# Kernel optimization log

Measured on AMD Instinct MI355X. Metric: run time of the kernel, lower is better.

The kernel has to match this reference:

```python
import jax, jax.numpy as jnp
import numpy as np

INPUT_SIZE = 32      # activity vocab
HIDDEN = 128
OUTPUT = 33          # 32 act logits + 1 duration
NUM_LAYERS = 2
MAX_LEN = 256
SOS = 0


def setup_inputs() -> dict:
    key = jax.random.key(0)
    ks = jax.random.split(key, 16)
    s = 0.05
    inp = {
        "batch_size": 8192,
        "hidden": jax.random.normal(ks[0], (NUM_LAYERS, 8192, HIDDEN), jnp.float32),
        # CustomEmbedding: embed act index to hidden-1 dims, concat raw duration -> hidden dims
        "emb": jax.random.normal(ks[1], (INPUT_SIZE, HIDDEN - 1), jnp.float32) * s,
        # torch.nn.GRU params, gate order (r, z, n)
        "w_ih_0": jax.random.normal(ks[2], (3 * HIDDEN, HIDDEN), jnp.float32) * s,
        "w_hh_0": jax.random.normal(ks[3], (3 * HIDDEN, HIDDEN), jnp.float32) * s,
        "b_ih_0": jax.random.normal(ks[4], (3 * HIDDEN,), jnp.float32) * s,
        "b_hh_0": jax.random.normal(ks[5], (3 * HIDDEN,), jnp.float32) * s,
        "w_ih_1": jax.random.normal(ks[6], (3 * HIDDEN, HIDDEN), jnp.float32) * s,
        "w_hh_1": jax.random.normal(ks[7], (3 * HIDDEN, HIDDEN), jnp.float32) * s,
        "b_ih_1": jax.random.normal(ks[8], (3 * HIDDEN,), jnp.float32) * s,
        "b_hh_1": jax.random.normal(ks[9], (3 * HIDDEN,), jnp.float32) * s,
        "fc_w": jax.random.normal(ks[10], (OUTPUT, HIDDEN), jnp.float32) * s,
        "fc_b": jax.random.normal(ks[11], (OUTPUT,), jnp.float32) * s,
    }
    return inp


def _gru_cell(x, h, w_ih, w_hh, b_ih, b_hh):
    gi = x @ w_ih.T + b_ih          # [B, 3H]
    gh = h @ w_hh.T + b_hh
    ir, iz, inn = jnp.split(gi, 3, axis=-1)
    hr, hz, hn = jnp.split(gh, 3, axis=-1)
    r = jax.nn.sigmoid(ir + hr)
    z = jax.nn.sigmoid(iz + hz)
    n = jnp.tanh(inn + r * hn)
    return (1.0 - z) * n + z * h


def _decode(batch_size, hidden, emb, w_ih_0, w_hh_0, b_ih_0, b_hh_0,
            w_ih_1, w_hh_1, b_ih_1, b_hh_1, fc_w, fc_b):
    B = batch_size
    # decoder_input [B, 2]: (act_index_as_float, duration); sos index = 0
    init_inp = jnp.zeros((B, 2), hidden.dtype).at[:, 0].set(float(SOS))

    def step(carry, _):
        inp, h = carry
        act = inp[:, 0].astype(jnp.int32)
        x = jnp.concatenate([emb[act], inp[:, 1:2]], axis=-1)   # [B, H]
        h0 = _gru_cell(x, h[0], w_ih_0, w_hh_0, b_ih_0, b_hh_0)
        h1 = _gru_cell(h0, h[1], w_ih_1, w_hh_1, b_ih_1, b_hh_1)
        pred = h1 @ fc_w.T + fc_b                                # [B, O]
        # pack(): argmax over act logits; softmax over a size-1 seq dim == 1.0
        topi = jnp.argmax(pred[:, : OUTPUT - 1], axis=-1)
        nxt = jnp.concatenate(
            [topi.astype(pred.dtype)[:, None], jnp.ones((B, 1), pred.dtype)], axis=-1)
        return (nxt, jnp.stack([h0, h1])), pred

    _, outs = jax.lax.scan(step, (init_inp, hidden), None, length=MAX_LEN)
    outs = jnp.transpose(outs, (1, 0, 2))                        # [B, T, O]
    acts_logits = outs[..., : OUTPUT - 1]
    durations = jax.nn.softmax(outs[..., OUTPUT - 1:], axis=1)   # softmax over time
    log_probs = jnp.concatenate(
        [jax.nn.log_softmax(acts_logits, axis=-1), durations], axis=-1)
    probs = jnp.concatenate(
        [jax.nn.softmax(acts_logits, axis=-1), durations], axis=-1)
    return log_probs, probs


def reference(batch_size, hidden, emb, w_ih_0, w_hh_0, b_ih_0, b_hh_0,
              w_ih_1, w_hh_1, b_ih_1, b_hh_1, fc_w, fc_b):
    return _decode(batch_size, hidden, emb, w_ih_0, w_hh_0, b_ih_0, b_hh_0,
                   w_ih_1, w_hh_1, b_ih_1, b_hh_1, fc_w, fc_b)
```

## Files before the change

### kernel.cpp

```cpp
#include <hip/hip_runtime.h>

#define HDIM  128
#define G3    384
#define RPB   32
#define NTHR  512
#define NSTEP 256
#define NOUT  33
#define BROWS 8192
#define NBLK  (BROWS / RPB)
#define LOGP_ELEMS 69206016LL

typedef _Float16 half8 __attribute__((ext_vector_type(8)));
typedef float    f32x4 __attribute__((ext_vector_type(4)));

#define HS0_OFF   0
#define HS1_OFF   16384
#define BST_OFF   32768
#define FCL_OFF   131072
#define LDS_BYTES 155648

#define WP_BYTES  294912
#define FP_BYTES  24576

__device__ __forceinline__ float sigf(float x) { return 1.0f / (1.0f + __expf(-x)); }
__device__ __forceinline__ float tanh_fast(float x) { return 1.0f - 2.0f / (__expf(2.0f*x) + 1.0f); }

__global__ void prep_kernel(const float* __restrict__ emb, const float* __restrict__ wih0,
                            const float* __restrict__ bih0, float* __restrict__ T1,
                            float* __restrict__ T0) {
    int a = blockIdx.x;
    int g = threadIdx.x;
    const float* e = emb + a * 127;
    const float* w = wih0 + g * HDIM;
    float s = bih0[g];
    for (int k = 0; k < 127; ++k) s += e[k] * w[k];
    T1[a * G3 + g] = s + w[127];
    if (a == 0) T0[g] = s;
}

__global__ void prep_pack(const float* __restrict__ whh0, const float* __restrict__ wih1,
                          const float* __restrict__ whh1, const float* __restrict__ fcw,
                          half8* __restrict__ WP) {
    int b = blockIdx.x;
    int tid  = threadIdx.x;
    int lane = tid & 63;
    int kc   = tid >> 6;
    bool isfc = (b >= 72);
    if (!isfc) {
        int mat = b / 24, nt = b % 24;
        const float* W = (mat == 0) ? whh0 : (mat == 1) ? wih1 : whh1;
        int g = nt * 16 + (lane & 15);
        int k = kc * 32 + (lane >> 4) * 8;
        half8 v1;
#pragma unroll
        for (int e = 0; e < 8; ++e) v1[e] = (_Float16)W[g * HDIM + k + e];
        WP[(size_t)(((mat * 24 + nt) * 4 + kc)) * 64 + lane] = v1;
    } else {
        int nt = b - 72;
        int g = nt * 16 + (lane & 15);
        int k = kc * 32 + (lane >> 4) * 8;
        half8 v1, v2;
#pragma unroll
        for (int e = 0; e < 8; ++e) {
            float x = (g >= NOUT) ? 0.0f : fcw[g * HDIM + k + e];
            _Float16 s1 = (_Float16)x;
            v1[e] = s1; v2[e] = (_Float16)(x - (float)s1);
        }
        size_t base = (size_t)(WP_BYTES / 1024 + (nt * 4 + kc) * 2) * 64 + lane;
        WP[base]      = v1;
        WP[base + 64] = v2;
    }
}

__launch_bounds__(NTHR, 2)
__global__ void decoder_kernel(const float* __restrict__ hid,
                               const float* __restrict__ T1, const float* __restrict__ T0,
                               const char* __restrict__ Bpg,
                               const float* __restrict__ bhh0,
                               const float* __restrict__ bih1, const float* __restrict__ bhh1,
                               const float* __restrict__ fcb,
                               float* __restrict__ out) {
    extern __shared__ char smraw[];
    char*  hs0 = smraw + HS0_OFF;
    char*  hs1 = smraw + HS1_OFF;
    char*  bst = smraw + BST_OFF;
    char*  fcl = smraw + FCL_OFF;

    const int tid  = threadIdx.x;
    const int row0 = blockIdx.x * RPB;
    float* lp = out;
    float* pp = out + LOGP_ELEMS;

    const int lane  = tid & 63;
    const int w     = tid >> 6;
    const int col   = lane & 15;
    const int q     = lane >> 4;
    const int akoff = q * 16;
    const int j     = w * 16 + col;
    char* const mybuf = bst + (size_t)w * 12288;

    const float bG0 = bhh0[j],       bG1 = bhh0[128 + j], bG2 = bhh0[256 + j];
    const float bH0 = bhh1[j],       bH1 = bhh1[128 + j], bH2 = bhh1[256 + j];
    const float bI0 = bih1[j],       bI1 = bih1[128 + j], bI2 = bih1[256 + j];

    f32x4 fcbr[3];
#pragma unroll
    for (int t2 = 0; t2 < 3; ++t2)
#pragma unroll
        for (int i = 0; i < 4; ++i) {
            int o = 16 * t2 + q * 4 + i;
            fcbr[t2][i] = (o < NOUT) ? fcb[o] : 0.0f;
        }

    {
        const uint4* src = (const uint4*)(Bpg + WP_BYTES);
        uint4* dst = (uint4*)fcl;
        for (int i = tid; i < FP_BYTES / 16; i += NTHR) dst[i] = src[i];
    }

    float h0v[2][4], h1v[2][4];
#pragma unroll
    for (int Mt = 0; Mt < 2; ++Mt)
#pragma unroll
        for (int i = 0; i < 4; ++i) {
            int row = Mt * 16 + q * 4 + i;
            float v0 = hid[(size_t)(row0 + row) * HDIM + j];
            float v1 = hid[(size_t)BROWS * HDIM + (size_t)(row0 + row) * HDIM + j];
            h0v[Mt][i] = v0; h1v[Mt][i] = v1;
            int off = (row * 256 + j * 2) ^ ((row & 7) << 4);
            _Float16 s1 = (_Float16)v0, s2 = (_Float16)(v0 - (float)s1);
            *(_Float16*)(hs0 + off) = s1;
            *(_Float16*)(hs0 + 8192 + off) = s2;
            s1 = (_Float16)v1; s2 = (_Float16)(v1 - (float)s1);
            *(_Float16*)(hs1 + off) = s1;
            *(_Float16*)(hs1 + 8192 + off) = s2;
        }
    __syncthreads();

#define LGKM0() asm volatile("s_waitcnt lgkmcnt(0)" ::: "memory")
#define VMW()   asm volatile("s_waitcnt vmcnt(9)" ::: "memory")
#define BAR()   __builtin_amdgcn_s_barrier()
#define MFMA(a, b, c) __builtin_amdgcn_mfma_f32_16x16x32_f16((a), (b), (c), 0, 0, 0)

#define STAGE3(G_) do {                                                           \
        int gm_  = (G_) % 12;                                                     \
        int mat_ = (gm_ < 4) ? 0 : ((gm_ < 8) ? 2 : 1);                           \
        int kc_  = gm_ & 3;                                                       \
        char* db_ = mybuf + (size_t)(3 * ((G_) & 3)) * 1024;                      \
        _Pragma("unroll")                                                         \
        for (int ty_ = 0; ty_ < 3; ++ty_) {                                       \
            const char* src_ = Bpg + (size_t)(((mat_ * 24 + (ty_ * 8 + w)) * 4 + kc_) * 1024) + lane * 16; \
            __builtin_amdgcn_global_load_lds((const unsigned int*)src_,           \
                                             (unsigned int*)(db_ + ty_ * 1024), 16, 0, 0); \
        }                                                                         \
    } while (0)

#define GROUP(G_, HS_, ACC_) do {                                                 \
        STAGE3((G_) + 3);                                                         \
        VMW();                                                                    \
        int kc_ = (G_) & 3;                                                       \
        half8 a1_[2], a2_[2];                                                     \
        _Pragma("unroll")                                                         \
        for (int Mt_ = 0; Mt_ < 2; ++Mt_) {                                       \
            int row_ = Mt_ * 16 + col;                                            \
            int off_ = (row_ * 256 + kc_ * 64 + akoff) ^ ((row_ & 7) << 4);       \
            a1_[Mt_] = *(const half8*)((HS_) + off_);                             \
            a2_[Mt_] = *(const half8*)((HS_) + 8192 + off_);                      \
        }                                                                         \
        char* db_ = mybuf + (size_t)(3 * ((G_) & 3)) * 1024;                      \
        half8 b0_ = *(const half8*)(db_ + lane * 16);                             \
        half8 b1_ = *(const half8*)(db_ + 1024 + lane * 16);                      \
        half8 b2_ = *(const half8*)(db_ + 2048 + lane * 16);                      \
        _Pragma("unroll")                                                         \
        for (int Mt_ = 0; Mt_ < 2; ++Mt_) {                                       \
            ACC_[0][Mt_] = MFMA(a1_[Mt_], b0_, ACC_[0][Mt_]);                     \
            ACC_[0][Mt_] = MFMA(a2_[Mt_], b0_, ACC_[0][Mt_]);                     \
        }                                                                         \
        _Pragma("unroll")                                                         \
        for (int Mt_ = 0; Mt_ < 2; ++Mt_) {                                       \
            ACC_[1][Mt_] = MFMA(a1_[Mt_], b1_, ACC_[1][Mt_]);                     \
            ACC_[1][Mt_] = MFMA(a2_[Mt_], b1_, ACC_[1][Mt_]);                     \
        }                                                                         \
        _Pragma("unroll")                                                         \
        for (int Mt_ = 0; Mt_ < 2; ++Mt_) {                                       \
            ACC_[2][Mt_] = MFMA(a1_[Mt_], b2_, ACC_[2][Mt_]);                     \
            ACC_[2][Mt_] = MFMA(a2_[Mt_], b2_, ACC_[2][Mt_]);                     \
        }                                                                         \
    } while (0)

#define FC_SOFTMAX(TOUT_, ACTS_) do {                                             \
        f32x4 facc[2][3];                                                         \
        _Pragma("unroll")                                                         \
        for (int Mt_ = 0; Mt_ < 2; ++Mt_)                                         \
            _Pragma("unroll")                                                     \
            for (int t2_ = 0; t2_ < 3; ++t2_) facc[Mt_][t2_] = fcbr[t2_];         \
        _Pragma("unroll")                                                         \
        for (int kc_ = 0; kc_ < 4; ++kc_) {                                       \
            half8 a1_[2], a2_[2];                                                 \
            _Pragma("unroll")                                                     \
            for (int Mt_ = 0; Mt_ < 2; ++Mt_) {                                   \
                int row_ = Mt_ * 16 + col;                                        \
                int off_ = (row_ * 256 + kc_ * 64 + akoff) ^ ((row_ & 7) << 4);   \
                a1_[Mt_] = *(const half8*)(hs1 + off_);                           \
                a2_[Mt_] = *(const half8*)(hs1 + 8192 + off_);                    \
            }                                                                     \
            _Pragma("unroll")                                                     \
            for (int t2_ = 0; t2_ < 3; ++t2_) {                                   \
                half8 f1_ = *(const half8*)(fcl + ((t2_ * 4 + kc_) * 2 + 0) * 1024 + lane * 16); \
                half8 f2_ = *(const half8*)(fcl + ((t2_ * 4 + kc_) * 2 + 1) * 1024 + lane * 16); \
                _Pragma("unroll")                                                 \
                for (int Mt_ = 0; Mt_ < 2; ++Mt_) {                               \
                    facc[Mt_][t2_] = MFMA(f1_, a1_[Mt_], facc[Mt_][t2_]);         \
                    facc[Mt_][t2_] = MFMA(f1_, a2_[Mt_], facc[Mt_][t2_]);         \
                    facc[Mt_][t2_] = MFMA(f2_, a1_[Mt_], facc[Mt_][t2_]);         \
                }                                                                 \
            }                                                                     \
        }                                                                         \
        _Pragma("unroll")                                                         \
        for (int Mt_ = 0; Mt_ < 2; ++Mt_) {                                       \
            float bv_ = facc[Mt_][0][0]; int bi_ = q * 4;                         \
            _Pragma("unroll")                                                     \
            for (int t2_ = 0; t2_ < 2; ++t2_)                                     \
                _Pragma("unroll")                                                 \
                for (int i_ = 0; i_ < 4; ++i_) {                                  \
                    if (t2_ == 0 && i_ == 0) continue;                            \
                    float v_ = facc[Mt_][t2_][i_];                                \
                    int   o_ = 16 * t2_ + q * 4 + i_;                             \
                    if (v_ > bv_) { bv_ = v_; bi_ = o_; }                         \
                }                                                                 \
            _Pragma("unroll")                                                     \
            for (int d_ = 16; d_ <= 32; d_ <<= 1) {                               \
                float ov_ = __shfl_xor(bv_, d_);                                  \
                int   oi_ = __shfl_xor(bi_, d_);                                  \
                if (ov_ > bv_ || (ov_ == bv_ && oi_ < bi_)) { bv_ = ov_; bi_ = oi_; } \
            }                                                                     \
            (ACTS_)[Mt_] = bi_;                                                   \
            if (w == Mt_) {                                                       \
                float ex_[2][4]; float s_ = 0.0f;                                 \
                _Pragma("unroll")                                                 \
                for (int t2_ = 0; t2_ < 2; ++t2_)                                 \
                    _Pragma("unroll")                                             \
                    for (int i_ = 0; i_ < 4; ++i_) {                              \
                        ex_[t2_][i_] = __expf(facc[Mt_][t2_][i_] - bv_);          \
                        s_ += ex_[t2_][i_];                                       \
                    }                                                             \
                s_ += __shfl_xor(s_, 16);                                         \
                s_ += __shfl_xor(s_, 32);                                         \
                float ls_ = __logf(s_), inv_ = 1.0f / s_;                         \
                int r_ = lane & 15;                                               \
                size_t base_ = ((size_t)(row0 + Mt_ * 16 + r_) * NSTEP + (TOUT_)) * NOUT; \
                _Pragma("unroll")                                                 \
                for (int t2_ = 0; t2_ < 2; ++t2_)                                 \
                    _Pragma("unroll")                                             \
                    for (int i_ = 0; i_ < 4; ++i_) {                              \
                        int o_ = 16 * t2_ + q * 4 + i_;                           \
                        lp[base_ + o_] = facc[Mt_][t2_][i_] - bv_ - ls_;          \
                        pp[base_ + o_] = ex_[t2_][i_] * inv_;                     \
                    }                                                             \
                if (q == 0) lp[base_ + 32] = facc[Mt_][2][0];                     \
            }                                                                     \
        }                                                                         \
    } while (0)

    STAGE3(0); STAGE3(1); STAGE3(2);

#pragma unroll 1
    for (int t = 0; t < NSTEP; ++t) {
        float gi[3][2][4];
        if (t == 0) {
            float g0v = T0[j], g1v = T0[128 + j], g2v = T0[256 + j];
#pragma unroll
            for (int Mt = 0; Mt < 2; ++Mt)
#pragma unroll
                for (int i = 0; i < 4; ++i) {
                    gi[0][Mt][i] = g0v; gi[1][Mt][i] = g1v; gi[2][Mt][i] = g2v;
                }
        } else {
            int actsR[2];
            FC_SOFTMAX(t - 1, actsR);
#pragma unroll
            for (int Mt = 0; Mt < 2; ++Mt)
#pragma unroll
                for (int i = 0; i < 4; ++i) {
                    int act = __shfl(actsR[Mt], q * 4 + i);
                    const float* tab = T1 + act * G3;
                    gi[0][Mt][i] = tab[j];
                    gi[1][Mt][i] = tab[128 + j];
                    gi[2][Mt][i] = tab[256 + j];
                }
        }

        f32x4 g0[3][2], ah[3][2];
        {
            f32x4 v0 = {bG0, bG0, bG0, bG0}, v1 = {bG1, bG1, bG1, bG1}, v2 = {bG2, bG2, bG2, bG2};
            g0[0][0] = v0; g0[0][1] = v0; g0[1][0] = v1; g0[1][1] = v1; g0[2][0] = v2; g0[2][1] = v2;
            f32x4 u0 = {bH0, bH0, bH0, bH0}, u1 = {bH1, bH1, bH1, bH1}, u2 = {bH2, bH2, bH2, bH2};
            ah[0][0] = u0; ah[0][1] = u0; ah[1][0] = u1; ah[1][1] = u1; ah[2][0] = u2; ah[2][1] = u2;
        }
        GROUP(0, hs0, g0); GROUP(1, hs0, g0); GROUP(2, hs0, g0); GROUP(3, hs0, g0);
        GROUP(4, hs1, ah); GROUP(5, hs1, ah);

        _Float16 s1r[2][4], s2r[2][4];
#pragma unroll
        for (int Mt = 0; Mt < 2; ++Mt)
#pragma unroll
            for (int i = 0; i < 4; ++i) {
                float rg = sigf(gi[0][Mt][i] + g0[0][Mt][i]);
                float zg = sigf(gi[1][Mt][i] + g0[1][Mt][i]);
                float ng = tanh_fast(gi[2][Mt][i] + rg * g0[2][Mt][i]);
                float hnew = (1.0f - zg) * ng + zg * h0v[Mt][i];
                h0v[Mt][i] = hnew;
                s1r[Mt][i] = (_Float16)hnew;
                s2r[Mt][i] = (_Float16)(hnew - (float)s1r[Mt][i]);
            }

        GROUP(6, hs1, ah); GROUP(7, hs1, ah);
        LGKM0(); BAR();

#pragma unroll
        for (int Mt = 0; Mt < 2; ++Mt)
#pragma unroll
            for (int i = 0; i < 4; ++i) {
                int row = Mt * 16 + q * 4 + i;
                int off = (row * 256 + j * 2) ^ ((row & 7) << 4);
                *(_Float16*)(hs0 + off) = s1r[Mt][i];
                *(_Float16*)(hs0 + 8192 + off) = s2r[Mt][i];
            }
        LGKM0(); BAR();

        f32x4 ai[3][2];
        {
            f32x4 v0 = {bI0, bI0, bI0, bI0}, v1 = {bI1, bI1, bI1, bI1}, v2 = {bI2, bI2, bI2, bI2};
            ai[0][0] = v0; ai[0][1] = v0; ai[1][0] = v1; ai[1][1] = v1; ai[2][0] = v2; ai[2][1] = v2;
        }
        GROUP(8, hs0, ai); GROUP(9, hs0, ai); GROUP(10, hs0, ai); GROUP(11, hs0, ai);

#pragma unroll
        for (int Mt = 0; Mt < 2; ++Mt)
#pragma unroll
            for (int i = 0; i < 4; ++i) {
                float rg = sigf(ai[0][Mt][i] + ah[0][Mt][i]);
                float zg = sigf(ai[1][Mt][i] + ah[1][Mt][i]);
                float ng = tanh_fast(ai[2][Mt][i] + rg * ah[2][Mt][i]);
                float hnew = (1.0f - zg) * ng + zg * h1v[Mt][i];
                h1v[Mt][i] = hnew;
                int row = Mt * 16 + q * 4 + i;
                int off = (row * 256 + j * 2) ^ ((row & 7) << 4);
                _Float16 s1 = (_Float16)hnew, s2 = (_Float16)(hnew - (float)s1);
                *(_Float16*)(hs1 + off) = s1;
                *(_Float16*)(hs1 + 8192 + off) = s2;
            }
        LGKM0(); BAR();
    }

    {
        int actsF[2];
        FC_SOFTMAX(NSTEP - 1, actsF);
        (void)actsF;
    }
#undef STAGE3
#undef GROUP
#undef FC_SOFTMAX
#undef LGKM0
#undef VMW
#undef BAR
#undef MFMA
}

__global__ void dur_kernel(float* __restrict__ out) {
    int wid  = threadIdx.x >> 6;
    int lane = threadIdx.x & 63;
    int row  = blockIdx.x * 4 + wid;
    float* lp = out;
    float* pp = out + LOGP_ELEMS;
    size_t base = (size_t)row * NSTEP * NOUT + 32;

    float v[4]; float m = -1e30f;
#pragma unroll
    for (int i = 0; i < 4; ++i) {
        v[i] = lp[base + (size_t)(lane * 4 + i) * NOUT];
        m = fmaxf(m, v[i]);
    }
#pragma unroll
    for (int d = 1; d < 64; d <<= 1) m = fmaxf(m, __shfl_xor(m, d));
    float e[4]; float s = 0.0f;
#pragma unroll
    for (int i = 0; i < 4; ++i) { e[i] = __expf(v[i] - m); s += e[i]; }
#pragma unroll
    for (int d = 1; d < 64; d <<= 1) s += __shfl_xor(s, d);
    float inv = 1.0f / s;
#pragma unroll
    for (int i = 0; i < 4; ++i) {
        size_t idx = base + (size_t)(lane * 4 + i) * NOUT;
        float dv = e[i] * inv;
        lp[idx] = dv;
        pp[idx] = dv;
    }
}

extern "C" void kernel_launch(void* const* d_in, const int* in_sizes, int n_in,
                              void* d_out, int out_size, void* d_ws, size_t ws_size,
                              hipStream_t stream) {
    const float* hid  = (const float*)d_in[1];
    const float* emb  = (const float*)d_in[2];
    const float* wih0 = (const float*)d_in[3];
    const float* whh0 = (const float*)d_in[4];
    const float* bih0 = (const float*)d_in[5];
    const float* bhh0 = (const float*)d_in[6];
    const float* wih1 = (const float*)d_in[7];
    const float* whh1 = (const float*)d_in[8];
    const float* bih1 = (const float*)d_in[9];
    const float* bhh1 = (const float*)d_in[10];
    const float* fcw  = (const float*)d_in[11];
    const float* fcb  = (const float*)d_in[12];

    char*  ws = (char*)d_ws;
    half8* WP = (half8*)ws;
    float* T1 = (float*)(ws + WP_BYTES + FP_BYTES);
    float* T0 = T1 + 32 * G3;

    prep_kernel<<<32, 384, 0, stream>>>(emb, wih0, bih0, T1, T0);
    prep_pack<<<75, 256, 0, stream>>>(whh0, wih1, whh1, fcw, WP);

    hipFuncSetAttribute((const void*)decoder_kernel,
                        hipFuncAttributeMaxDynamicSharedMemorySize, LDS_BYTES);
    decoder_kernel<<<NBLK, NTHR, LDS_BYTES, stream>>>(
        hid, T1, T0, ws, bhh0, bih1, bhh1, fcb, (float*)d_out);

    dur_kernel<<<BROWS / 4, 256, 0, stream>>>((float*)d_out);
}
```

Measured before the change: 2.674 ms.

## Split each block's row tiles across twice as many waves

Doubles the block size to 1024 threads so each wave handles one 16-row M tile instead of two. The per-wave B-staging ring shrinks from four slots to two (prefetch distance 1, adjusted vmcnt), and the FC/argmax work is also split per M tile. Both M-tile waves now stream the same weight tiles, doubling global-to-LDS weight traffic per block. It also shortens the latency each wave can hide with its prefetch.

After: 4.756 ms. 1.78x slower.

```diff
diff --git a/kernel.cpp b/kernel.cpp
--- a/kernel.cpp
+++ b/kernel.cpp
@@ -3,7 +3,7 @@
 #define HDIM  128
 #define G3    384
 #define RPB   32
-#define NTHR  512
+#define NTHR  1024
 #define NSTEP 256
 #define NOUT  33
 #define BROWS 8192
@@ -72,7 +72,7 @@
     }
 }
 
-__launch_bounds__(NTHR, 2)
+__launch_bounds__(NTHR, 4)
 __global__ void decoder_kernel(const float* __restrict__ hid,
                                const float* __restrict__ T1, const float* __restrict__ T0,
                                const char* __restrict__ Bpg,
@@ -93,15 +93,17 @@
 
     const int lane  = tid & 63;
     const int w     = tid >> 6;
+    const int wcol  = w & 7;
+    const int Mt    = w >> 3;
     const int col   = lane & 15;
     const int q     = lane >> 4;
     const int akoff = q * 16;
-    const int j     = w * 16 + col;
-    char* const mybuf = bst + (size_t)w * 12288;
-
-    const float bG0 = bhh0[j],       bG1 = bhh0[128 + j], bG2 = bhh0[256 + j];
-    const float bH0 = bhh1[j],       bH1 = bhh1[128 + j], bH2 = bhh1[256 + j];
-    const float bI0 = bih1[j],       bI1 = bih1[128 + j], bI2 = bih1[256 + j];
+    const int j     = wcol * 16 + col;
+    char* const mybuf = bst + (size_t)w * 6144;
+
+    const float bG0 = bhh0[j], bG1 = bhh0[128 + j], bG2 = bhh0[256 + j];
+    const float bH0 = bhh1[j], bH1 = bhh1[128 + j], bH2 = bhh1[256 + j];
+    const float bI0 = bih1[j], bI1 = bih1[128 + j], bI2 = bih1[256 + j];
 
     f32x4 fcbr[3];
 #pragma unroll
@@ -118,27 +120,25 @@
         for (int i = tid; i < FP_BYTES / 16; i += NTHR) dst[i] = src[i];
     }
 
-    float h0v[2][4], h1v[2][4];
-#pragma unroll
-    for (int Mt = 0; Mt < 2; ++Mt)
-#pragma unroll
-        for (int i = 0; i < 4; ++i) {
-            int row = Mt * 16 + q * 4 + i;
-            float v0 = hid[(size_t)(row0 + row) * HDIM + j];
-            float v1 = hid[(size_t)BROWS * HDIM + (size_t)(row0 + row) * HDIM + j];
-            h0v[Mt][i] = v0; h1v[Mt][i] = v1;
-            int off = (row * 256 + j * 2) ^ ((row & 7) << 4);
-            _Float16 s1 = (_Float16)v0, s2 = (_Float16)(v0 - (float)s1);
-            *(_Float16*)(hs0 + off) = s1;
-            *(_Float16*)(hs0 + 8192 + off) = s2;
-            s1 = (_Float16)v1; s2 = (_Float16)(v1 - (float)s1);
-            *(_Float16*)(hs1 + off) = s1;
-            *(_Float16*)(hs1 + 8192 + off) = s2;
-        }
+    float h0v[4], h1v[4];
+#pragma unroll
+    for (int i = 0; i < 4; ++i) {
+        int row = Mt * 16 + q * 4 + i;
+        float v0 = hid[(size_t)(row0 + row) * HDIM + j];
+        float v1 = hid[(size_t)BROWS * HDIM + (size_t)(row0 + row) * HDIM + j];
+        h0v[i] = v0; h1v[i] = v1;
+        int off = (row * 256 + j * 2) ^ ((row & 7) << 4);
+        _Float16 s1 = (_Float16)v0, s2 = (_Float16)(v0 - (float)s1);
+        *(_Float16*)(hs0 + off) = s1;
+        *(_Float16*)(hs0 + 8192 + off) = s2;
+        s1 = (_Float16)v1; s2 = (_Float16)(v1 - (float)s1);
+        *(_Float16*)(hs1 + off) = s1;
+        *(_Float16*)(hs1 + 8192 + off) = s2;
+    }
     __syncthreads();
 
 #define LGKM0() asm volatile("s_waitcnt lgkmcnt(0)" ::: "memory")
-#define VMW()   asm volatile("s_waitcnt vmcnt(9)" ::: "memory")
+#define VMW()   asm volatile("s_waitcnt vmcnt(3)" ::: "memory")
 #define BAR()   __builtin_amdgcn_s_barrier()
 #define MFMA(a, b, c) __builtin_amdgcn_mfma_f32_16x16x32_f16((a), (b), (c), 0, 0, 0)
 
@@ -146,85 +146,62 @@
         int gm_  = (G_) % 12;                                                     \
         int mat_ = (gm_ < 4) ? 0 : ((gm_ < 8) ? 2 : 1);                           \
         int kc_  = gm_ & 3;                                                       \
-        char* db_ = mybuf + (size_t)(3 * ((G_) & 3)) * 1024;                      \
+        char* db_ = mybuf + (size_t)(3 * ((G_) & 1)) * 1024;                      \
         _Pragma("unroll")                                                         \
         for (int ty_ = 0; ty_ < 3; ++ty_) {                                       \
-            const char* src_ = Bpg + (size_t)(((mat_ * 24 + (ty_ * 8 + w)) * 4 + kc_) * 1024) + lane * 16; \
+            const char* src_ = Bpg + (size_t)(((mat_ * 24 + (ty_ * 8 + wcol)) * 4 + kc_) * 1024) + lane * 16; \
             __builtin_amdgcn_global_load_lds((const unsigned int*)src_,           \
                                              (unsigned int*)(db_ + ty_ * 1024), 16, 0, 0); \
         }                                                                         \
     } while (0)
 
 #define GROUP(G_, HS_, ACC_) do {                                                 \
-        STAGE3((G_) + 3);                                                         \
+        STAGE3((G_) + 1);                                                         \
         VMW();                                                                    \
         int kc_ = (G_) & 3;                                                       \
-        half8 a1_[2], a2_[2];                                                     \
-        _Pragma("unroll")                                                         \
-        for (int Mt_ = 0; Mt_ < 2; ++Mt_) {                                       \
-            int row_ = Mt_ * 16 + col;                                            \
-            int off_ = (row_ * 256 + kc_ * 64 + akoff) ^ ((row_ & 7) << 4);       \
-            a1_[Mt_] = *(const half8*)((HS_) + off_);                             \
-            a2_[Mt_] = *(const half8*)((HS_) + 8192 + off_);                      \
-        }                                                                         \
-        char* db_ = mybuf + (size_t)(3 * ((G_) & 3)) * 1024;                      \
+        int row_ = Mt * 16 + col;                                                 \
+        int off_ = (row_ * 256 + kc_ * 64 + akoff) ^ ((row_ & 7) << 4);           \
+        half8 a1_ = *(const half8*)((HS_) + off_);                                \
+        half8 a2_ = *(const half8*)((HS_) + 8192 + off_);                         \
+        char* db_ = mybuf + (size_t)(3 * ((G_) & 1)) * 1024;                      \
         half8 b0_ = *(const half8*)(db_ + lane * 16);                             \
         half8 b1_ = *(const half8*)(db_ + 1024 + lane * 16);                      \
         half8 b2_ = *(const half8*)(db_ + 2048 + lane * 16);                      \
+        ACC_[0] = MFMA(a1_, b0_, ACC_[0]);                                        \
+        ACC_[0] = MFMA(a2_, b0_, ACC_[0]);                                        \
+        ACC_[1] = MFMA(a1_, b1_, ACC_[1]);                                        \
+        ACC_[1] = MFMA(a2_, b1_, ACC_[1]);                                        \
+        ACC_[2] = MFMA(a1_, b2_, ACC_[2]);                                        \
+        ACC_[2] = MFMA(a2_, b2_, ACC_[2]);                                        \
+    } while (0)
+
+#define FC_SOFTMAX(TOUT_, ACTS_) do {                                             \
+        f32x4 facc[3];                                                            \
         _Pragma("unroll")                                                         \
-        for (int Mt_ = 0; Mt_ < 2; ++Mt_) {                                       \
-            ACC_[0][Mt_] = MFMA(a1_[Mt_], b0_, ACC_[0][Mt_]);                     \
-            ACC_[0][Mt_] = MFMA(a2_[Mt_], b0_, ACC_[0][Mt_]);                     \
-        }                                                                         \
-        _Pragma("unroll")                                                         \
-        for (int Mt_ = 0; Mt_ < 2; ++Mt_) {                                       \
-            ACC_[1][Mt_] = MFMA(a1_[Mt_], b1_, ACC_[1][Mt_]);                     \
-            ACC_[1][Mt_] = MFMA(a2_[Mt_], b1_, ACC_[1][Mt_]);                     \
-        }                                                                         \
-        _Pragma("unroll")                                                         \
-        for (int Mt_ = 0; Mt_ < 2; ++Mt_) {                                       \
-            ACC_[2][Mt_] = MFMA(a1_[Mt_], b2_, ACC_[2][Mt_]);                     \
-            ACC_[2][Mt_] = MFMA(a2_[Mt_], b2_, ACC_[2][Mt_]);                     \
-        }                                                                         \
-    } while (0)
-
-#define FC_SOFTMAX(TOUT_, ACTS_) do {                                             \
-        f32x4 facc[2][3];                                                         \
-        _Pragma("unroll")                                                         \
-        for (int Mt_ = 0; Mt_ < 2; ++Mt_)                                         \
-            _Pragma("unroll")                                                     \
-            for (int t2_ = 0; t2_ < 3; ++t2_) facc[Mt_][t2_] = fcbr[t2_];         \
+        for (int t2_ = 0; t2_ < 3; ++t2_) facc[t2_] = fcbr[t2_];                  \
         _Pragma("unroll")                                                         \
         for (int kc_ = 0; kc_ < 4; ++kc_) {                                       \
-            half8 a1_[2], a2_[2];                                                 \
-            _Pragma("unroll")                                                     \
-            for (int Mt_ = 0; Mt_ < 2; ++Mt_) {                                   \
-                int row_ = Mt_ * 16 + col;                                        \
-                int off_ = (row_ * 256 + kc_ * 64 + akoff) ^ ((row_ & 7) << 4);   \
-                a1_[Mt_] = *(const half8*)(hs1 + off_);                           \
-                a2_[Mt_] = *(const half8*)(hs1 + 8192 + off_);                    \
-            }                                                                     \
+            int row_ = Mt * 16 + col;                                             \
+            int off_ = (row_ * 256 + kc_ * 64 + akoff) ^ ((row_ & 7) << 4);       \
+            half8 a1_ = *(const half8*)(hs1 + off_);                              \
+            half8 a2_ = *(const half8*)(hs1 + 8192 + off_);                       \
             _Pragma("unroll")                                                     \
             for (int t2_ = 0; t2_ < 3; ++t2_) {                                   \
                 half8 f1_ = *(const half8*)(fcl + ((t2_ * 4 + kc_) * 2 + 0) * 1024 + lane * 16); \
                 half8 f2_ = *(const half8*)(fcl + ((t2_ * 4 + kc_) * 2 + 1) * 1024 + lane * 16); \
-                _Pragma("unroll")                                                 \
-                for (int Mt_ = 0; Mt_ < 2; ++Mt_) {                               \
-                    facc[Mt_][t2_] = MFMA(f1_, a1_[Mt_], facc[Mt_][t2_]);         \
-                    facc[Mt_][t2_] = MFMA(f1_, a2_[Mt_], facc[Mt_][t2_]);         \
-                    facc[Mt_][t2_] = MFMA(f2_, a1_[Mt_], facc[Mt_][t2_]);         \
-                }                                                                 \
+                facc[t2_] = MFMA(f1_, a1_, facc[t2_]);                            \
+                facc[t2_] = MFMA(f1_, a2_, facc[t2_]);                            \
+                facc[t2_] = MFMA(f2_, a1_, facc[t2_]);                            \
             }                                                                     \
         }                                                                         \
-        _Pragma("unroll")                                                         \
-        for (int Mt_ = 0; Mt_ < 2; ++Mt_) {                                       \
-            float bv_ = facc[Mt_][0][0]; int bi_ = q * 4;                         \
+        {                                                                         \
+            float bv_ = facc[0][0]; int bi_ = q * 4;                              \
             _Pragma("unroll")                                                     \
             for (int t2_ = 0; t2_ < 2; ++t2_)                                     \
                 _Pragma("unroll")                                                 \
                 for (int i_ = 0; i_ < 4; ++i_) {                                  \
                     if (t2_ == 0 && i_ == 0) continue;                            \
-                    float v_ = facc[Mt_][t2_][i_];                                \
+                    float v_ = facc[t2_][i_];                                     \
                     int   o_ = 16 * t2_ + q * 4 + i_;                             \
                     if (v_ > bv_) { bv_ = v_; bi_ = o_; }                         \
                 }                                                                 \
@@ -234,127 +211,117 @@
                 int   oi_ = __shfl_xor(bi_, d_);                                  \
                 if (ov_ > bv_ || (ov_ == bv_ && oi_ < bi_)) { bv_ = ov_; bi_ = oi_; } \
             }                                                                     \
-            (ACTS_)[Mt_] = bi_;                                                   \
-            if (w == Mt_) {                                                       \
+            (ACTS_) = bi_;                                                        \
+            if (wcol == 0) {                                                      \
                 float ex_[2][4]; float s_ = 0.0f;                                 \
                 _Pragma("unroll")                                                 \
                 for (int t2_ = 0; t2_ < 2; ++t2_)                                 \
                     _Pragma("unroll")                                             \
                     for (int i_ = 0; i_ < 4; ++i_) {                              \
-                        ex_[t2_][i_] = __expf(facc[Mt_][t2_][i_] - bv_);          \
+                        ex_[t2_][i_] = __expf(facc[t2_][i_] - bv_);               \
                         s_ += ex_[t2_][i_];                                       \
                     }                                                             \
                 s_ += __shfl_xor(s_, 16);                                         \
                 s_ += __shfl_xor(s_, 32);                                         \
                 float ls_ = __logf(s_), inv_ = 1.0f / s_;                         \
                 int r_ = lane & 15;                                               \
-                size_t base_ = ((size_t)(row0 + Mt_ * 16 + r_) * NSTEP + (TOUT_)) * NOUT; \
+                size_t base_ = ((size_t)(row0 + Mt * 16 + r_) * NSTEP + (TOUT_)) * NOUT; \
                 _Pragma("unroll")                                                 \
                 for (int t2_ = 0; t2_ < 2; ++t2_)                                 \
                     _Pragma("unroll")                                             \
                     for (int i_ = 0; i_ < 4; ++i_) {                              \
                         int o_ = 16 * t2_ + q * 4 + i_;                           \
-                        lp[base_ + o_] = facc[Mt_][t2_][i_] - bv_ - ls_;          \
+                        lp[base_ + o_] = facc[t2_][i_] - bv_ - ls_;               \
                         pp[base_ + o_] = ex_[t2_][i_] * inv_;                     \
                     }                                                             \
-                if (q == 0) lp[base_ + 32] = facc[Mt_][2][0];                     \
+                if (q == 0) lp[base_ + 32] = facc[2][0];                          \
             }                                                                     \
         }                                                                         \
     } while (0)
 
-    STAGE3(0); STAGE3(1); STAGE3(2);
+    STAGE3(0);
 
 #pragma unroll 1
     for (int t = 0; t < NSTEP; ++t) {
-        float gi[3][2][4];
+        float gi[3][4];
         if (t == 0) {
             float g0v = T0[j], g1v = T0[128 + j], g2v = T0[256 + j];
 #pragma unroll
-            for (int Mt = 0; Mt < 2; ++Mt)
-#pragma unroll
-                for (int i = 0; i < 4; ++i) {
-                    gi[0][Mt][i] = g0v; gi[1][Mt][i] = g1v; gi[2][Mt][i] = g2v;
-                }
+            for (int i = 0; i < 4; ++i) {
+                gi[0][i] = g0v; gi[1][i] = g1v; gi[2][i] = g2v;
+            }
         } else {
-            int actsR[2];
+            int actsR;
             FC_SOFTMAX(t - 1, actsR);
 #pragma unroll
-            for (int Mt = 0; Mt < 2; ++Mt)
-#pragma unroll
-                for (int i = 0; i < 4; ++i) {
-                    int act = __shfl(actsR[Mt], q * 4 + i);
-                    const float* tab = T1 + act * G3;
-                    gi[0][Mt][i] = tab[j];
-                    gi[1][Mt][i] = tab[128 + j];
-                    gi[2][Mt][i] = tab[256 + j];
-                }
-        }
-
-        f32x4 g0[3][2], ah[3][2];
+            for (int i = 0; i < 4; ++i) {
+                int act = __shfl(actsR, q * 4 + i);
+                const float* tab = T1 + act * G3;
+                gi[0][i] = tab[j];
+                gi[1][i] = tab[128 + j];
+                gi[2][i] = tab[256 + j];
+            }
+        }
+
+        f32x4 g0[3], ah[3];
         {
             f32x4 v0 = {bG0, bG0, bG0, bG0}, v1 = {bG1, bG1, bG1, bG1}, v2 = {bG2, bG2, bG2, bG2};
-            g0[0][0] = v0; g0[0][1] = v0; g0[1][0] = v1; g0[1][1] = v1; g0[2][0] = v2; g0[2][1] = v2;
+            g0[0] = v0; g0[1] = v1; g0[2] = v2;
             f32x4 u0 = {bH0, bH0, bH0, bH0}, u1 = {bH1, bH1, bH1, bH1}, u2 = {bH2, bH2, bH2, bH2};
-            ah[0][0] = u0; ah[0][1] = u0; ah[1][0] = u1; ah[1][1] = u1; ah[2][0] = u2; ah[2][1] = u2;
+            ah[0] = u0; ah[1] = u1; ah[2] = u2;
         }
         GROUP(0, hs0, g0); GROUP(1, hs0, g0); GROUP(2, hs0, g0); GROUP(3, hs0, g0);
         GROUP(4, hs1, ah); GROUP(5, hs1, ah);
 
-        _Float16 s1r[2][4], s2r[2][4];
-#pragma unroll
-        for (int Mt = 0; Mt < 2; ++Mt)
-#pragma unroll
-            for (int i = 0; i < 4; ++i) {
-                float rg = sigf(gi[0][Mt][i] + g0[0][Mt][i]);
-                float zg = sigf(gi[1][Mt][i] + g0[1][Mt][i]);
-                float ng = tanh_fast(gi[2][Mt][i] + rg * g0[2][Mt][i]);
-                float hnew = (1.0f - zg) * ng + zg * h0v[Mt][i];
-                h0v[Mt][i] = hnew;
-                s1r[Mt][i] = (_Float16)hnew;
-                s2r[Mt][i] = (_Float16)(hnew - (float)s1r[Mt][i]);
-            }
+        _Float16 s1r[4], s2r[4];
+#pragma unroll
+        for (int i = 0; i < 4; ++i) {
+            float rg = sigf(gi[0][i] + g0[0][i]);
+            float zg = sigf(gi[1][i] + g0[1][i]);
+            float ng = tanh_fast(gi[2][i] + rg * g0[2][i]);
+            float hnew = (1.0f - zg) * ng + zg * h0v[i];
+            h0v[i] = hnew;
+            s1r[i] = (_Float16)hnew;
+            s2r[i] = (_Float16)(hnew - (float)s1r[i]);
+        }
 
         GROUP(6, hs1, ah); GROUP(7, hs1, ah);
         LGKM0(); BAR();
 
 #pragma unroll
-        for (int Mt = 0; Mt < 2; ++Mt)
-#pragma unroll
-            for (int i = 0; i < 4; ++i) {
-                int row = Mt * 16 + q * 4 + i;
-                int off = (row * 256 + j * 2) ^ ((row & 7) << 4);
-                *(_Float16*)(hs0 + off) = s1r[Mt][i];
-                *(_Float16*)(hs0 + 8192 + off) = s2r[Mt][i];
-            }
+        for (int i = 0; i < 4; ++i) {
+            int row = Mt * 16 + q * 4 + i;
+            int off = (row * 256 + j * 2) ^ ((row & 7) << 4);
+            *(_Float16*)(hs0 + off) = s1r[i];
+            *(_Float16*)(hs0 + 8192 + off) = s2r[i];
+        }
         LGKM0(); BAR();
 
-        f32x4 ai[3][2];
+        f32x4 ai[3];
         {
             f32x4 v0 = {bI0, bI0, bI0, bI0}, v1 = {bI1, bI1, bI1, bI1}, v2 = {bI2, bI2, bI2, bI2};
-            ai[0][0] = v0; ai[0][1] = v0; ai[1][0] = v1; ai[1][1] = v1; ai[2][0] = v2; ai[2][1] = v2;
+            ai[0] = v0; ai[1] = v1; ai[2] = v2;
         }
         GROUP(8, hs0, ai); GROUP(9, hs0, ai); GROUP(10, hs0, ai); GROUP(11, hs0, ai);
 
 #pragma unroll
-        for (int Mt = 0; Mt < 2; ++Mt)
-#pragma unroll
-            for (int i = 0; i < 4; ++i) {
-                float rg = sigf(ai[0][Mt][i] + ah[0][Mt][i]);
-                float zg = sigf(ai[1][Mt][i] + ah[1][Mt][i]);
-                float ng = tanh_fast(ai[2][Mt][i] + rg * ah[2][Mt][i]);
-                float hnew = (1.0f - zg) * ng + zg * h1v[Mt][i];
-                h1v[Mt][i] = hnew;
-                int row = Mt * 16 + q * 4 + i;
-                int off = (row * 256 + j * 2) ^ ((row & 7) << 4);
-                _Float16 s1 = (_Float16)hnew, s2 = (_Float16)(hnew - (float)s1);
-                *(_Float16*)(hs1 + off) = s1;
-                *(_Float16*)(hs1 + 8192 + off) = s2;
-            }
+        for (int i = 0; i < 4; ++i) {
+            float rg = sigf(ai[0][i] + ah[0][i]);
+            float zg = sigf(ai[1][i] + ah[1][i]);
+            float ng = tanh_fast(ai[2][i] + rg * ah[2][i]);
+            float hnew = (1.0f - zg) * ng + zg * h1v[i];
+            h1v[i] = hnew;
+            int row = Mt * 16 + q * 4 + i;
+            int off = (row * 256 + j * 2) ^ ((row & 7) << 4);
+            _Float16 s1 = (_Float16)hnew, s2 = (_Float16)(hnew - (float)s1);
+            *(_Float16*)(hs1 + off) = s1;
+            *(_Float16*)(hs1 + 8192 + off) = s2;
+        }
         LGKM0(); BAR();
     }
 
     {
-        int actsF[2];
+        int actsF;
         FC_SOFTMAX(NSTEP - 1, actsF);
         (void)actsF;
     }
```
